# Optimization experiments

Measured on AMD Instinct MI355X. Metric: run time of the kernel, lower is better.

The kernel has to match this reference:

```python
import jax, jax.numpy as jnp
import numpy as np
from jax import lax


def _conv(x, w, b):
    # x: [B,C,H,W] NCHW, w: [O,I,3,3] OIHW, SAME padding, stride 1
    y = lax.conv_general_dilated(x, w, (1, 1), 'SAME',
                                 dimension_numbers=('NCHW', 'OIHW', 'NCHW'))
    return y + b[None, :, None, None]


def _maxpool2(x):
    return lax.reduce_window(x, -jnp.inf, lax.max,
                             (1, 1, 2, 2), (1, 1, 2, 2), 'VALID')


def _squash(x):
    # x: [..., D]
    norm = jnp.sum(x * x, axis=-1, keepdims=True)
    scale = norm / (1.0 + norm) / jnp.sqrt(norm + 1e-9)
    return scale * x


def _routing(x, W):
    # x: [B, R, C]  (R routes, C in_channels); W: [N, R, C, O]
    # u_hat[b,n,r,o] = sum_c x[b,r,c] * W[n,r,c,o]
    u_hat = jnp.einsum('brc,nrco->bnro', x, W)
    B, N, R, O = u_hat.shape
    b_ij = jnp.zeros((B, N, R), dtype=u_hat.dtype)
    v = None
    for it in range(3):  # fixed 3 routing iterations
        c_ij = jax.nn.softmax(b_ij, axis=2)
        s_j = jnp.einsum('bnr,bnro->bno', c_ij, u_hat)
        v = _squash(s_j)
        if it < 2:
            b_ij = b_ij + jnp.einsum('bnro,bno->bnr', u_hat, v)
    return v  # [B, N, O]


def setup_inputs() -> dict:
    key = jax.random.key(0)
    ks = jax.random.split(key, 10)
    B = 512
    num_classes = 15
    x = jax.random.normal(ks[0], (B, 3, 64, 64), dtype=jnp.float32)

    def kaiming(k, shape, fan_in):
        return jax.random.normal(k, shape, dtype=jnp.float32) * np.sqrt(2.0 / fan_in)

    w1 = kaiming(ks[1], (8, 3, 3, 3), 3 * 9)
    b1 = jnp.zeros((8,), jnp.float32)
    w2 = kaiming(ks[2], (16, 8, 3, 3), 8 * 9)
    b2 = jnp.zeros((16,), jnp.float32)
    w3 = kaiming(ks[3], (32, 16, 3, 3), 16 * 9)
    b3 = jnp.zeros((32,), jnp.float32)
    # route_weights are torch.randn in the original (std 1.0)
    rw1 = jax.random.normal(ks[4], (32, 64, 32, 8), dtype=jnp.float32)   # primary
    rw2 = jax.random.normal(ks[5], (num_classes, 32, 8, 16), dtype=jnp.float32)  # secondary
    fc_w = kaiming(ks[6], (num_classes, 16 * num_classes), 16 * num_classes)
    fc_b = jnp.zeros((num_classes,), jnp.float32)
    return {'x': x, 'w1': w1, 'b1': b1, 'w2': w2, 'b2': b2,
            'w3': w3, 'b3': b3, 'rw1': rw1, 'rw2': rw2,
            'fc_w': fc_w, 'fc_b': fc_b}


def reference(x, w1, b1, w2, b2, w3, b3, rw1, rw2, fc_w, fc_b):
    h = _maxpool2(jax.nn.relu(_conv(x, w1, b1)))   # [B,8,32,32]
    h = _maxpool2(jax.nn.relu(_conv(h, w2, b2)))   # [B,16,16,16]
    h = _maxpool2(jax.nn.relu(_conv(h, w3, b3)))   # [B,32,8,8]
    B = h.shape[0]
    # routes = 64 spatial positions, channels = 32 capsule input features
    feats = h.reshape(B, 32, 64).transpose(0, 2, 1)  # [B, 64, 32]
    v1 = _routing(feats, rw1)   # [B, 32, 8]
    v2 = _routing(v1, rw2)      # [B, 15, 16]
    flat = v2.reshape(B, -1)    # [B, 240]
    return flat @ fc_w.T + fc_b  # [B, 15]
```

## Files before the change

### kernel.cpp

```cpp
#include <hip/hip_runtime.h>
#include <hip/hip_bf16.h>


__global__ __launch_bounds__(256)
void conv_stack(const float* __restrict__ x,
                const float* __restrict__ w1g, const float* __restrict__ b1g,
                const float* __restrict__ w2g, const float* __restrict__ b2g,
                const float* __restrict__ w3g, const float* __restrict__ b3g,
                float* __restrict__ h3)
{
    __shared__ float lds[18152];
    float* A  = lds;
    float* o1 = lds + 6936;
    float* w3 = lds + 6936;
    float* o3 = lds + 11544;
    float* w1 = lds + 16728;
    float* w2 = lds + 16944;
    float* bb = lds + 18096;

    const int tid = threadIdx.x;
    const int b   = blockIdx.x;

    {
        float4 z = make_float4(0.f, 0.f, 0.f, 0.f);
        for (int i = tid; i < 4182; i += 256) ((float4*)lds)[i] = z;
        for (int i = tid; i < 216; i += 256) {
            int o = i % 8, k = (i / 8) % 9, c = i / 72;
            w1[i] = w1g[(o * 3 + c) * 9 + k];
        }
        for (int i = tid; i < 1152; i += 256) {
            int o = i % 16, k = (i / 16) % 9, c = i / 144;
            w2[i] = w2g[(o * 8 + c) * 9 + k];
        }
        if (tid < 8)  bb[tid]      = b1g[tid];
        if (tid < 16) bb[8 + tid]  = b2g[tid];
        if (tid < 32) bb[24 + tid] = b3g[tid];
    }
    const float4* gin = (const float4*)(x + (size_t)b * 3 * 64 * 64);

    auto stage_band = [&](int y0) {
        for (int i = tid; i < 3 * 34 * 16; i += 256) {
            int ch = i % 16;
            int ly = (i / 16) % 34;
            int c  = i / (16 * 34);
            int y  = y0 + ly;
            float4 v = make_float4(0.f, 0.f, 0.f, 0.f);
            if (y >= 0 && y < 64) v = gin[(c * 64 + y) * 16 + ch];
            float* d = &A[(c * 34 + ly) * 68 + 1 + ch * 4];
            d[0] = v.x; d[1] = v.y; d[2] = v.z; d[3] = v.w;
        }
    };
    stage_band(-1);
    __syncthreads();

    auto conv1_band = [&](int band) {
        const int s  = tid & 7;
        const int py = (tid >> 3) & 15;
        const int og = tid >> 7;
        const int X0 = 8 * s;
        float acc[4][2][8];
#pragma unroll
        for (int n = 0; n < 4; ++n)
#pragma unroll
            for (int q = 0; q < 2; ++q)
#pragma unroll
                for (int j = 0; j < 8; ++j) acc[n][q][j] = 0.f;
#pragma unroll
        for (int c = 0; c < 3; ++c) {
            float rows[4][12];
#pragma unroll
            for (int rr = 0; rr < 4; ++rr) {
                const float4* src = (const float4*)&A[(c * 34 + 2 * py + rr) * 68 + X0];
#pragma unroll
                for (int j = 0; j < 3; ++j) {
                    float4 v = src[j];
                    rows[rr][j * 4 + 0] = v.x; rows[rr][j * 4 + 1] = v.y;
                    rows[rr][j * 4 + 2] = v.z; rows[rr][j * 4 + 3] = v.w;
                }
            }
            const float* wc = w1 + c * 72;
#pragma unroll
            for (int ky = 0; ky < 3; ++ky)
#pragma unroll
                for (int n = 0; n < 4; ++n) {
                    const float q0 = wc[(ky * 3 + 0) * 8 + og * 4 + n];
                    const float q1 = wc[(ky * 3 + 1) * 8 + og * 4 + n];
                    const float q2 = wc[(ky * 3 + 2) * 8 + og * 4 + n];
#pragma unroll
                    for (int j = 0; j < 8; ++j) {
                        acc[n][0][j] = fmaf(rows[ky][j],     q0, acc[n][0][j]);
                        acc[n][0][j] = fmaf(rows[ky][j + 1], q1, acc[n][0][j]);
                        acc[n][0][j] = fmaf(rows[ky][j + 2], q2, acc[n][0][j]);
                        acc[n][1][j] = fmaf(rows[ky + 1][j],     q0, acc[n][1][j]);
                        acc[n][1][j] = fmaf(rows[ky + 1][j + 1], q1, acc[n][1][j]);
                        acc[n][1][j] = fmaf(rows[ky + 1][j + 2], q2, acc[n][1][j]);
                    }
                }
        }
#pragma unroll
        for (int n = 0; n < 4; ++n) {
            const float bv = bb[og * 4 + n];
            const int row = 1 + band * 16 + py;
#pragma unroll
            for (int j = 0; j < 4; ++j) {
                float m = fmaxf(fmaxf(acc[n][0][2 * j], acc[n][0][2 * j + 1]),
                                fmaxf(acc[n][1][2 * j], acc[n][1][2 * j + 1]));
                o1[((og * 4 + n) * 34 + row) * 36 + 1 + 4 * s + j] = fmaxf(m + bv, 0.f);
            }
        }
    };
    conv1_band(0);
    __syncthreads();
    stage_band(31);
    __syncthreads();
    conv1_band(1);
    __syncthreads();

    {
        float4 z = make_float4(0.f, 0.f, 0.f, 0.f);
        for (int i = tid; i < 1734; i += 256) ((float4*)A)[i] = z;
    }
    __syncthreads();

    {
        const int s  = tid & 3;
        const int py = (tid >> 2) & 15;
        const int og = tid >> 6;
        const int X0 = 8 * s;
        float acc[4][2][8];
#pragma unroll
        for (int n = 0; n < 4; ++n)
#pragma unroll
            for (int q = 0; q < 2; ++q)
#pragma unroll
                for (int j = 0; j < 8; ++j) acc[n][q][j] = 0.f;
        for (int c = 0; c < 8; ++c) {
            float rows[4][12];
#pragma unroll
            for (int rr = 0; rr < 4; ++rr) {
                const float4* src = (const float4*)&o1[(c * 34 + 2 * py + rr) * 36 + X0];
#pragma unroll
                for (int j = 0; j < 3; ++j) {
                    float4 v = src[j];
                    rows[rr][j * 4 + 0] = v.x; rows[rr][j * 4 + 1] = v.y;
                    rows[rr][j * 4 + 2] = v.z; rows[rr][j * 4 + 3] = v.w;
                }
            }
            const float* wc = w2 + c * 144;
#pragma unroll
            for (int ky = 0; ky < 3; ++ky)
#pragma unroll
                for (int n = 0; n < 4; ++n) {
                    const float q0 = wc[(ky * 3 + 0) * 16 + og * 4 + n];
                    const float q1 = wc[(ky * 3 + 1) * 16 + og * 4 + n];
                    const float q2 = wc[(ky * 3 + 2) * 16 + og * 4 + n];
#pragma unroll
                    for (int j = 0; j < 8; ++j) {
                        acc[n][0][j] = fmaf(rows[ky][j],     q0, acc[n][0][j]);
                        acc[n][0][j] = fmaf(rows[ky][j + 1], q1, acc[n][0][j]);
                        acc[n][0][j] = fmaf(rows[ky][j + 2], q2, acc[n][0][j]);
                        acc[n][1][j] = fmaf(rows[ky + 1][j],     q0, acc[n][1][j]);
                        acc[n][1][j] = fmaf(rows[ky + 1][j + 1], q1, acc[n][1][j]);
                        acc[n][1][j] = fmaf(rows[ky + 1][j + 2], q2, acc[n][1][j]);
                    }
                }
        }
#pragma unroll
        for (int n = 0; n < 4; ++n) {
            const float bv = bb[8 + og * 4 + n];
#pragma unroll
            for (int j = 0; j < 4; ++j) {
                float m = fmaxf(fmaxf(acc[n][0][2 * j], acc[n][0][2 * j + 1]),
                                fmaxf(acc[n][1][2 * j], acc[n][1][2 * j + 1]));
                A[((og * 4 + n) * 18 + 1 + py) * 20 + 1 + 4 * s + j] = fmaxf(m + bv, 0.f);
            }
        }
    }
    __syncthreads();

    for (int i = tid; i < 4608; i += 256) {
        int o = i % 32, k = (i / 32) % 9, c = i / 288;
        w3[i] = w3g[(o * 16 + c) * 9 + k];
    }
    __syncthreads();

    {
        const int s  = tid & 1;
        const int py = (tid >> 1) & 7;
        const int og = tid >> 4;
        const int X0 = 8 * s;
        float acc[2][2][8];
#pragma unroll
        for (int n = 0; n < 2; ++n)
#pragma unroll
            for (int q = 0; q < 2; ++q)
#pragma unroll
                for (int j = 0; j < 8; ++j) acc[n][q][j] = 0.f;
        for (int c = 0; c < 16; ++c) {
            float rows[4][12];
#pragma unroll
            for (int rr = 0; rr < 4; ++rr) {
                const float4* src = (const float4*)&A[(c * 18 + 2 * py + rr) * 20 + X0];
#pragma unroll
                for (int j = 0; j < 3; ++j) {
                    float4 v = src[j];
                    rows[rr][j * 4 + 0] = v.x; rows[rr][j * 4 + 1] = v.y;
                    rows[rr][j * 4 + 2] = v.z; rows[rr][j * 4 + 3] = v.w;
                }
            }
            const float* wc = w3 + c * 288;
#pragma unroll
            for (int ky = 0; ky < 3; ++ky)
#pragma unroll
                for (int n = 0; n < 2; ++n) {
                    const float q0 = wc[(ky * 3 + 0) * 32 + og * 2 + n];
                    const float q1 = wc[(ky * 3 + 1) * 32 + og * 2 + n];
                    const float q2 = wc[(ky * 3 + 2) * 32 + og * 2 + n];
#pragma unroll
                    for (int j = 0; j < 8; ++j) {
                        acc[n][0][j] = fmaf(rows[ky][j],     q0, acc[n][0][j]);
                        acc[n][0][j] = fmaf(rows[ky][j + 1], q1, acc[n][0][j]);
                        acc[n][0][j] = fmaf(rows[ky][j + 2], q2, acc[n][0][j]);
                        acc[n][1][j] = fmaf(rows[ky + 1][j],     q0, acc[n][1][j]);
                        acc[n][1][j] = fmaf(rows[ky + 1][j + 1], q1, acc[n][1][j]);
                        acc[n][1][j] = fmaf(rows[ky + 1][j + 2], q2, acc[n][1][j]);
                    }
                }
        }
#pragma unroll
        for (int n = 0; n < 2; ++n) {
            const float bv = bb[24 + og * 2 + n];
            float4 ov;
            float* p = (float*)&ov;
#pragma unroll
            for (int j = 0; j < 4; ++j) {
                float m = fmaxf(fmaxf(acc[n][0][2 * j], acc[n][0][2 * j + 1]),
                                fmaxf(acc[n][1][2 * j], acc[n][1][2 * j + 1]));
                p[j] = fmaxf(m + bv, 0.f);
            }
            *(float4*)&o3[(og * 2 + n) * 64 + py * 8 + 4 * s] = ov;
        }
    }
    __syncthreads();

    {
        float4* dst = (float4*)(h3 + (size_t)b * 2048);
        const float4* src = (const float4*)o3;
        for (int i = tid; i < 512; i += 256) dst[i] = src[i];
    }
}

__global__ __launch_bounds__(256)
void transpose_w1(const float* __restrict__ W, float* __restrict__ Wt)
{
    int idx = blockIdx.x * 256 + threadIdx.x;
    if (idx >= 32 * 32 * 64 * 2) return;
    int half = idx & 1;
    int r    = (idx >> 1) & 63;
    int c    = (idx >> 7) & 31;
    int n    = idx >> 12;
    ((float4*)Wt)[idx] =
        ((const float4*)W)[(((n * 64 + r) * 32 + c) << 1) + half];
}

__global__ __launch_bounds__(256)
void routing1_einsum(const float* __restrict__ h3, const float* __restrict__ Wt,
                     float* __restrict__ uhat)
{
    constexpr int C = 32, R = 64, O = 8, G = 8;
    const int lane = threadIdx.x & 63;
    const int n    = blockIdx.y * 4 + (threadIdx.x >> 6);
    const int b0   = blockIdx.x * G;

    float u[G][O];
#pragma unroll
    for (int g = 0; g < G; ++g)
#pragma unroll
        for (int o = 0; o < O; ++o) u[g][o] = 0.f;

    const float4* wp = (const float4*)Wt + (size_t)n * C * R * 2;
    const float* xb = h3 + (size_t)b0 * (C * R) + lane;

#pragma unroll 4
    for (int c = 0; c < C; ++c) {
        float xv[G];
#pragma unroll
        for (int g = 0; g < G; ++g) xv[g] = xb[(size_t)g * (C * R) + c * R];
        float4 w0 = wp[(c * R + lane) * 2];
        float4 w1 = wp[(c * R + lane) * 2 + 1];
#pragma unroll
        for (int g = 0; g < G; ++g) {
            u[g][0] = fmaf(xv[g], w0.x, u[g][0]);
            u[g][1] = fmaf(xv[g], w0.y, u[g][1]);
            u[g][2] = fmaf(xv[g], w0.z, u[g][2]);
            u[g][3] = fmaf(xv[g], w0.w, u[g][3]);
            u[g][4] = fmaf(xv[g], w1.x, u[g][4]);
            u[g][5] = fmaf(xv[g], w1.y, u[g][5]);
            u[g][6] = fmaf(xv[g], w1.z, u[g][6]);
            u[g][7] = fmaf(xv[g], w1.w, u[g][7]);
        }
    }
#pragma unroll
    for (int g = 0; g < G; ++g) {
        float4* dst = (float4*)(uhat + (((size_t)(b0 + g) * 32 + n) * R + lane) * O);
        dst[0] = make_float4(u[g][0], u[g][1], u[g][2], u[g][3]);
        dst[1] = make_float4(u[g][4], u[g][5], u[g][6], u[g][7]);
    }
}

__global__ __launch_bounds__(256)
void routing1_iter(const float* __restrict__ uhat, float* __restrict__ v1)
{
    constexpr int O = 8;
    const int t  = threadIdx.x;
    const int b  = blockIdx.x;
    const int n  = t >> 3;
    const int rp = t & 7;

    float u[8][O];
    {
        const float4* up = (const float4*)(uhat + (((size_t)b * 32 + n) * 64 + rp * 8) * O);
#pragma unroll
        for (int i = 0; i < 16; ++i) {
            float4 w = up[i];
            u[i >> 1][(i & 1) * 4 + 0] = w.x;
            u[i >> 1][(i & 1) * 4 + 1] = w.y;
            u[i >> 1][(i & 1) * 4 + 2] = w.z;
            u[i >> 1][(i & 1) * 4 + 3] = w.w;
        }
    }

    float bij[8];
#pragma unroll
    for (int k = 0; k < 8; ++k) bij[k] = 0.f;
    float s[O];

#pragma unroll
    for (int it = 0; it < 3; ++it) {
        float e[8];
        float inv;
        if (it == 0) {
#pragma unroll
            for (int k = 0; k < 8; ++k) e[k] = 1.f;
            inv = 1.0f / 64.0f;
        } else {
            float mx = bij[0];
#pragma unroll
            for (int k = 1; k < 8; ++k) mx = fmaxf(mx, bij[k]);
#pragma unroll
            for (int m = 1; m < 8; m <<= 1) mx = fmaxf(mx, __shfl_xor(mx, m, 64));
            float sum = 0.f;
#pragma unroll
            for (int k = 0; k < 8; ++k) { e[k] = __expf(bij[k] - mx); sum += e[k]; }
#pragma unroll
            for (int m = 1; m < 8; m <<= 1) sum += __shfl_xor(sum, m, 64);
            inv = 1.f / sum;
        }
        float ta[O];
#pragma unroll
        for (int o = 0; o < O; ++o) ta[o] = 0.f;
#pragma unroll
        for (int k = 0; k < 8; ++k)
#pragma unroll
            for (int o = 0; o < O; ++o) ta[o] = fmaf(e[k], u[k][o], ta[o]);
#pragma unroll
        for (int m = 1; m < 8; m <<= 1)
#pragma unroll
            for (int o = 0; o < O; ++o) ta[o] += __shfl_xor(ta[o], m, 64);
        float nr = 0.f;
#pragma unroll
        for (int o = 0; o < O; ++o) { s[o] = ta[o] * inv; nr = fmaf(s[o], s[o], nr); }
        float scale = nr / (1.f + nr) / sqrtf(nr + 1e-9f);
#pragma unroll
        for (int o = 0; o < O; ++o) s[o] *= scale;
        if (it < 2) {
#pragma unroll
            for (int k = 0; k < 8; ++k) {
                float d = 0.f;
#pragma unroll
                for (int o = 0; o < O; ++o) d = fmaf(u[k][o], s[o], d);
                bij[k] += d;
            }
        }
    }
    float outv = s[0];
#pragma unroll
    for (int o = 1; o < O; ++o) outv = (rp == o) ? s[o] : outv;
    v1[(size_t)b * 256 + n * 8 + rp] = outv;
}

__global__ __launch_bounds__(256)
void routing2_fc(const float* __restrict__ v1, const float* __restrict__ W,
                 const float* __restrict__ fcw, const float* __restrict__ fcb,
                 float* __restrict__ out)
{
    constexpr int R = 32, C = 8, O = 16;
    __shared__ float vv[240];

    const int t  = threadIdx.x;
    const int b  = blockIdx.x;
    const int wv = t >> 6;
    const int lane = t & 63;
    const int nh = lane >> 5;
    const int r  = lane & 31;

    const float4* xr = (const float4*)(v1 + (size_t)b * 256 + r * 8);
    float4 x0 = xr[0], x1 = xr[1];
    float xv[8] = {x0.x, x0.y, x0.z, x0.w, x1.x, x1.y, x1.z, x1.w};

    float u[2][O];
    int nn[2];
#pragma unroll
    for (int p = 0; p < 2; ++p) {
        int n = wv * 4 + p * 2 + nh;
        nn[p] = n;
        int ncl = n < 15 ? n : 14;
        const float4* wp = (const float4*)(W + ((size_t)(ncl * R + r) * C) * O);
#pragma unroll
        for (int o = 0; o < O; ++o) u[p][o] = 0.f;
#pragma unroll
        for (int c = 0; c < C; ++c) {
#pragma unroll
            for (int j = 0; j < 4; ++j) {
                float4 w4 = wp[c * 4 + j];
                u[p][j * 4 + 0] = fmaf(xv[c], w4.x, u[p][j * 4 + 0]);
                u[p][j * 4 + 1] = fmaf(xv[c], w4.y, u[p][j * 4 + 1]);
                u[p][j * 4 + 2] = fmaf(xv[c], w4.z, u[p][j * 4 + 2]);
                u[p][j * 4 + 3] = fmaf(xv[c], w4.w, u[p][j * 4 + 3]);
            }
        }
    }

    float bij[2] = {0.f, 0.f};
    float s[2][O];
#pragma unroll
    for (int it = 0; it < 3; ++it) {
#pragma unroll
        for (int p = 0; p < 2; ++p) {
            float cc;
            if (it == 0) {
                cc = 1.0f / 32.0f;
            } else {
                float mx = bij[p];
#pragma unroll
                for (int w = 1; w < 32; w <<= 1) mx = fmaxf(mx, __shfl_xor(mx, w, 32));
                float e = __expf(bij[p] - mx);
                float sum = e;
#pragma unroll
                for (int w = 1; w < 32; w <<= 1) sum += __shfl_xor(sum, w, 32);
                cc = e / sum;
            }
#pragma unroll
            for (int o = 0; o < O; ++o) s[p][o] = cc * u[p][o];
        }
#pragma unroll
        for (int w = 1; w < 32; w <<= 1)
#pragma unroll
            for (int p = 0; p < 2; ++p)
#pragma unroll
                for (int o = 0; o < O; ++o) s[p][o] += __shfl_xor(s[p][o], w, 32);
#pragma unroll
        for (int p = 0; p < 2; ++p) {
            float nr = 0.f;
#pragma unroll
            for (int o = 0; o < O; ++o) nr = fmaf(s[p][o], s[p][o], nr);
            float scale = nr / (1.f + nr) / sqrtf(nr + 1e-9f);
#pragma unroll
            for (int o = 0; o < O; ++o) s[p][o] *= scale;
            if (it < 2) {
                float d = 0.f;
#pragma unroll
                for (int o = 0; o < O; ++o) d = fmaf(u[p][o], s[p][o], d);
                bij[p] += d;
            }
        }
    }
#pragma unroll
    for (int p = 0; p < 2; ++p) {
        float outv = 0.f;
#pragma unroll
        for (int o = 0; o < O; ++o) outv = (r == o) ? s[p][o] : outv;
        if (r < O && nn[p] < 15) vv[nn[p] * O + r] = outv;
    }
    __syncthreads();
    if (t < 240) {
        int j = t >> 4, k0 = t & 15;
        float acc = 0.f;
        for (int k = k0; k < 240; k += 16) acc = fmaf(vv[k], fcw[j * 240 + k], acc);
#pragma unroll
        for (int w = 1; w < 16; w <<= 1) acc += __shfl_xor(acc, w, 16);
        if (k0 == 0) out[(size_t)b * 15 + j] = acc + fcb[j];
    }
}

extern "C" void kernel_launch(void* const* d_in, const int* in_sizes, int n_in,
                              void* d_out, int out_size, void* d_ws, size_t ws_size,
                              hipStream_t stream) {
    const float* x    = (const float*)d_in[0];
    const float* w1   = (const float*)d_in[1];
    const float* b1   = (const float*)d_in[2];
    const float* w2   = (const float*)d_in[3];
    const float* b2   = (const float*)d_in[4];
    const float* w3   = (const float*)d_in[5];
    const float* b3   = (const float*)d_in[6];
    const float* rw1  = (const float*)d_in[7];
    const float* rw2  = (const float*)d_in[8];
    const float* fcw  = (const float*)d_in[9];
    const float* fcb  = (const float*)d_in[10];
    float* out = (float*)d_out;

    const int B = 512;
    float* ws = (float*)d_ws;
    float* uhat = ws;
    float* h3   = uhat + (size_t)8388608;
    float* v1   = h3 + (size_t)B * 32 * 8 * 8;
    float* Wt   = v1 + (size_t)B * 256;

    conv_stack<<<B, 256, 0, stream>>>(x, w1, b1, w2, b2, w3, b3, h3);
    transpose_w1<<<(32 * 32 * 64 * 2 + 255) / 256, 256, 0, stream>>>(rw1, Wt);
    {
        dim3 grid(B / 8, 8);
        routing1_einsum<<<grid, 256, 0, stream>>>(h3, Wt, uhat);
    }
    routing1_iter<<<B, 256, 0, stream>>>(uhat, v1);
    routing2_fc<<<B, 256, 0, stream>>>(v1, rw2, fcw, fcb, out);
}
```

Before: 199.1 us.

## Split conv stack per image into two row halves with halo recompute

```diff
diff --git a/kernel.cpp b/kernel.cpp
--- a/kernel.cpp
+++ b/kernel.cpp
@@ -3,27 +3,30 @@
 
 
 __global__ __launch_bounds__(256)
-void conv_stack(const float* __restrict__ x,
-                const float* __restrict__ w1g, const float* __restrict__ b1g,
-                const float* __restrict__ w2g, const float* __restrict__ b2g,
-                const float* __restrict__ w3g, const float* __restrict__ b3g,
-                float* __restrict__ h3)
+void conv_stack_h(const float* __restrict__ x,
+                  const float* __restrict__ w1g, const float* __restrict__ b1g,
+                  const float* __restrict__ w2g, const float* __restrict__ b2g,
+                  const float* __restrict__ w3g, const float* __restrict__ b3g,
+                  float* __restrict__ h3)
 {
-    __shared__ float lds[18152];
+    __shared__ float lds[11960];
     float* A  = lds;
-    float* o1 = lds + 6936;
-    float* w3 = lds + 6936;
-    float* o3 = lds + 11544;
-    float* w1 = lds + 16728;
-    float* w2 = lds + 16944;
-    float* bb = lds + 18096;
+    float* o2 = lds;
+    float* o1 = lds + 4488;
+    float* w3 = lds + 4488;
+    float* o3 = lds + 9096;
+    float* w1 = lds + 10536;
+    float* w2 = lds + 10752;
+    float* bb = lds + 11904;
 
     const int tid = threadIdx.x;
     const int b   = blockIdx.x;
+    const int h   = blockIdx.y;
+    const int base1 = h ? 12 : -1;
 
     {
         float4 z = make_float4(0.f, 0.f, 0.f, 0.f);
-        for (int i = tid; i < 4182; i += 256) ((float4*)lds)[i] = z;
+        for (int i = tid; i < 2634; i += 256) ((float4*)lds)[i] = z;
         for (int i = tid; i < 216; i += 256) {
             int o = i % 8, k = (i / 8) % 9, c = i / 72;
             w1[i] = w1g[(o * 3 + c) * 9 + k];
@@ -36,28 +39,104 @@
         if (tid < 16) bb[8 + tid]  = b2g[tid];
         if (tid < 32) bb[24 + tid] = b3g[tid];
     }
+    __syncthreads();
+
     const float4* gin = (const float4*)(x + (size_t)b * 3 * 64 * 64);
 
-    auto stage_band = [&](int y0) {
-        for (int i = tid; i < 3 * 34 * 16; i += 256) {
-            int ch = i % 16;
-            int ly = (i / 16) % 34;
-            int c  = i / (16 * 34);
-            int y  = y0 + ly;
+    auto stage_band = [&](int x0) {
+        for (int i = tid; i < 3 * 22 * 16; i += 256) {
+            int ch = i & 15;
+            int ly = (i >> 4) % 22;
+            int c  = i / (16 * 22);
+            int y  = x0 + ly;
             float4 v = make_float4(0.f, 0.f, 0.f, 0.f);
             if (y >= 0 && y < 64) v = gin[(c * 64 + y) * 16 + ch];
-            float* d = &A[(c * 34 + ly) * 68 + 1 + ch * 4];
+            float* d = &A[(c * 22 + ly) * 68 + 1 + ch * 4];
             d[0] = v.x; d[1] = v.y; d[2] = v.z; d[3] = v.w;
         }
     };
-    stage_band(-1);
-    __syncthreads();
-
-    auto conv1_band = [&](int band) {
-        const int s  = tid & 7;
-        const int py = (tid >> 3) & 15;
-        const int og = tid >> 7;
+
+    auto conv1_band = [&](int l_start, int nrows) {
+        const int NT = nrows * 16;
+        if (tid < NT) {
+            const int s  = tid & 7;
+            const int lr = (tid >> 3) % nrows;
+            const int og = tid / (8 * nrows);
+            const int X0 = 8 * s;
+            float acc[4][2][8];
+#pragma unroll
+            for (int n = 0; n < 4; ++n)
+#pragma unroll
+                for (int q = 0; q < 2; ++q)
+#pragma unroll
+                    for (int j = 0; j < 8; ++j) acc[n][q][j] = 0.f;
+#pragma unroll
+            for (int c = 0; c < 3; ++c) {
+                float rows[4][12];
+#pragma unroll
+                for (int rr = 0; rr < 4; ++rr) {
+                    const float4* src = (const float4*)&A[(c * 22 + 2 * lr + rr) * 68 + X0];
+#pragma unroll
+                    for (int j = 0; j < 3; ++j) {
+                        float4 v = src[j];
+                        rows[rr][j * 4 + 0] = v.x; rows[rr][j * 4 + 1] = v.y;
+                        rows[rr][j * 4 + 2] = v.z; rows[rr][j * 4 + 3] = v.w;
+                    }
+                }
+                const float* wc = w1 + c * 72;
+#pragma unroll
+                for (int ky = 0; ky < 3; ++ky)
+#pragma unroll
+                    for (int n = 0; n < 4; ++n) {
+                        const float q0 = wc[(ky * 3 + 0) * 8 + og * 4 + n];
+                        const float q1 = wc[(ky * 3 + 1) * 8 + og * 4 + n];
+                        const float q2 = wc[(ky * 3 + 2) * 8 + og * 4 + n];
+#pragma unroll
+                        for (int j = 0; j < 8; ++j) {
+                            acc[n][0][j] = fmaf(rows[ky][j],     q0, acc[n][0][j]);
+                            acc[n][0][j] = fmaf(rows[ky][j + 1], q1, acc[n][0][j]);
+                            acc[n][0][j] = fmaf(rows[ky][j + 2], q2, acc[n][0][j]);
+                            acc[n][1][j] = fmaf(rows[ky + 1][j],     q0, acc[n][1][j]);
+                            acc[n][1][j] = fmaf(rows[ky + 1][j + 1], q1, acc[n][1][j]);
+                            acc[n][1][j] = fmaf(rows[ky + 1][j + 2], q2, acc[n][1][j]);
+                        }
+                    }
+            }
+            const int l = l_start + lr;
+#pragma unroll
+            for (int n = 0; n < 4; ++n) {
+                const float bv = bb[og * 4 + n];
+#pragma unroll
+                for (int j = 0; j < 4; ++j) {
+                    float m = fmaxf(fmaxf(acc[n][0][2 * j], acc[n][0][2 * j + 1]),
+                                    fmaxf(acc[n][1][2 * j], acc[n][1][2 * j + 1]));
+                    o1[((og * 4 + n) * 21 + l) * 36 + 1 + 4 * s + j] = fmaxf(m + bv, 0.f);
+                }
+            }
+        }
+    };
+
+    stage_band(2 * base1 + 1);
+    __syncthreads();
+    conv1_band(1, 10);
+    __syncthreads();
+    stage_band(2 * base1 + 21);
+    __syncthreads();
+    conv1_band(11, 9);
+    __syncthreads();
+
+    {
+        float4 z = make_float4(0.f, 0.f, 0.f, 0.f);
+        for (int i = tid; i < 800; i += 256) ((float4*)o2)[i] = z;
+    }
+    __syncthreads();
+
+    if (tid < 144) {
+        const int s  = tid & 3;
+        const int jl = (tid >> 2) % 9;
+        const int og = tid / 36;
         const int X0 = 8 * s;
+        const int l2 = jl + 1 - h;
         float acc[4][2][8];
 #pragma unroll
         for (int n = 0; n < 4; ++n)
@@ -65,12 +144,11 @@
             for (int q = 0; q < 2; ++q)
 #pragma unroll
                 for (int j = 0; j < 8; ++j) acc[n][q][j] = 0.f;
-#pragma unroll
-        for (int c = 0; c < 3; ++c) {
+        for (int c = 0; c < 8; ++c) {
             float rows[4][12];
 #pragma unroll
             for (int rr = 0; rr < 4; ++rr) {
-                const float4* src = (const float4*)&A[(c * 34 + 2 * py + rr) * 68 + X0];
+                const float4* src = (const float4*)&o1[(c * 21 + 2 * jl + h + rr) * 36 + X0];
 #pragma unroll
                 for (int j = 0; j < 3; ++j) {
                     float4 v = src[j];
@@ -78,14 +156,14 @@
                     rows[rr][j * 4 + 2] = v.z; rows[rr][j * 4 + 3] = v.w;
                 }
             }
-            const float* wc = w1 + c * 72;
+            const float* wc = w2 + c * 144;
 #pragma unroll
             for (int ky = 0; ky < 3; ++ky)
 #pragma unroll
                 for (int n = 0; n < 4; ++n) {
-                    const float q0 = wc[(ky * 3 + 0) * 8 + og * 4 + n];
-                    const float q1 = wc[(ky * 3 + 1) * 8 + og * 4 + n];
-                    const float q2 = wc[(ky * 3 + 2) * 8 + og * 4 + n];
+                    const float q0 = wc[(ky * 3 + 0) * 16 + og * 4 + n];
+                    const float q1 = wc[(ky * 3 + 1) * 16 + og * 4 + n];
+                    const float q2 = wc[(ky * 3 + 2) * 16 + og * 4 + n];
 #pragma unroll
                     for (int j = 0; j < 8; ++j) {
                         acc[n][0][j] = fmaf(rows[ky][j],     q0, acc[n][0][j]);
@@ -99,46 +177,40 @@
         }
 #pragma unroll
         for (int n = 0; n < 4; ++n) {
-            const float bv = bb[og * 4 + n];
-            const int row = 1 + band * 16 + py;
+            const float bv = bb[8 + og * 4 + n];
 #pragma unroll
             for (int j = 0; j < 4; ++j) {
                 float m = fmaxf(fmaxf(acc[n][0][2 * j], acc[n][0][2 * j + 1]),
                                 fmaxf(acc[n][1][2 * j], acc[n][1][2 * j + 1]));
-                o1[((og * 4 + n) * 34 + row) * 36 + 1 + 4 * s + j] = fmaxf(m + bv, 0.f);
-            }
-        }
-    };
-    conv1_band(0);
-    __syncthreads();
-    stage_band(31);
-    __syncthreads();
-    conv1_band(1);
-    __syncthreads();
-
-    {
-        float4 z = make_float4(0.f, 0.f, 0.f, 0.f);
-        for (int i = tid; i < 1734; i += 256) ((float4*)A)[i] = z;
-    }
-    __syncthreads();
-
-    {
-        const int s  = tid & 3;
-        const int py = (tid >> 2) & 15;
-        const int og = tid >> 6;
+                o2[((og * 4 + n) * 10 + l2) * 20 + 1 + 4 * s + j] = fmaxf(m + bv, 0.f);
+            }
+        }
+    }
+    __syncthreads();
+
+    for (int i = tid; i < 4608; i += 256) {
+        int o = i % 32, k = (i / 32) % 9, c = i / 288;
+        w3[i] = w3g[(o * 16 + c) * 9 + k];
+    }
+    __syncthreads();
+
+    if (tid < 128) {
+        const int s  = tid & 1;
+        const int k  = (tid >> 1) & 3;
+        const int og = tid >> 3;
         const int X0 = 8 * s;
-        float acc[4][2][8];
-#pragma unroll
-        for (int n = 0; n < 4; ++n)
+        float acc[2][2][8];
+#pragma unroll
+        for (int n = 0; n < 2; ++n)
 #pragma unroll
             for (int q = 0; q < 2; ++q)
 #pragma unroll
                 for (int j = 0; j < 8; ++j) acc[n][q][j] = 0.f;
-        for (int c = 0; c < 8; ++c) {
+        for (int c = 0; c < 16; ++c) {
             float rows[4][12];
 #pragma unroll
             for (int rr = 0; rr < 4; ++rr) {
-                const float4* src = (const float4*)&o1[(c * 34 + 2 * py + rr) * 36 + X0];
+                const float4* src = (const float4*)&o2[(c * 10 + 2 * k + rr) * 20 + X0];
 #pragma unroll
                 for (int j = 0; j < 3; ++j) {
                     float4 v = src[j];
@@ -146,14 +218,14 @@
                     rows[rr][j * 4 + 2] = v.z; rows[rr][j * 4 + 3] = v.w;
                 }
             }
-            const float* wc = w2 + c * 144;
+            const float* wc = w3 + c * 288;
 #pragma unroll
             for (int ky = 0; ky < 3; ++ky)
 #pragma unroll
-                for (int n = 0; n < 4; ++n) {
-                    const float q0 = wc[(ky * 3 + 0) * 16 + og * 4 + n];
-                    const float q1 = wc[(ky * 3 + 1) * 16 + og * 4 + n];
-                    const float q2 = wc[(ky * 3 + 2) * 16 + og * 4 + n];
+                for (int n = 0; n < 2; ++n) {
+                    const float q0 = wc[(ky * 3 + 0) * 32 + og * 2 + n];
+                    const float q1 = wc[(ky * 3 + 1) * 32 + og * 2 + n];
+                    const float q2 = wc[(ky * 3 + 2) * 32 + og * 2 + n];
 #pragma unroll
                     for (int j = 0; j < 8; ++j) {
                         acc[n][0][j] = fmaf(rows[ky][j],     q0, acc[n][0][j]);
@@ -166,68 +238,6 @@
                 }
         }
 #pragma unroll
-        for (int n = 0; n < 4; ++n) {
-            const float bv = bb[8 + og * 4 + n];
-#pragma unroll
-            for (int j = 0; j < 4; ++j) {
-                float m = fmaxf(fmaxf(acc[n][0][2 * j], acc[n][0][2 * j + 1]),
-                                fmaxf(acc[n][1][2 * j], acc[n][1][2 * j + 1]));
-                A[((og * 4 + n) * 18 + 1 + py) * 20 + 1 + 4 * s + j] = fmaxf(m + bv, 0.f);
-            }
-        }
-    }
-    __syncthreads();
-
-    for (int i = tid; i < 4608; i += 256) {
-        int o = i % 32, k = (i / 32) % 9, c = i / 288;
-        w3[i] = w3g[(o * 16 + c) * 9 + k];
-    }
-    __syncthreads();
-
-    {
-        const int s  = tid & 1;
-        const int py = (tid >> 1) & 7;
-        const int og = tid >> 4;
-        const int X0 = 8 * s;
-        float acc[2][2][8];
-#pragma unroll
-        for (int n = 0; n < 2; ++n)
-#pragma unroll
-            for (int q = 0; q < 2; ++q)
-#pragma unroll
-                for (int j = 0; j < 8; ++j) acc[n][q][j] = 0.f;
-        for (int c = 0; c < 16; ++c) {
-            float rows[4][12];
-#pragma unroll
-            for (int rr = 0; rr < 4; ++rr) {
-                const float4* src = (const float4*)&A[(c * 18 + 2 * py + rr) * 20 + X0];
-#pragma unroll
-                for (int j = 0; j < 3; ++j) {
-                    float4 v = src[j];
-                    rows[rr][j * 4 + 0] = v.x; rows[rr][j * 4 + 1] = v.y;
-                    rows[rr][j * 4 + 2] = v.z; rows[rr][j * 4 + 3] = v.w;
-                }
-            }
-            const float* wc = w3 + c * 288;
-#pragma unroll
-            for (int ky = 0; ky < 3; ++ky)
-#pragma unroll
-                for (int n = 0; n < 2; ++n) {
-                    const float q0 = wc[(ky * 3 + 0) * 32 + og * 2 + n];
-                    const float q1 = wc[(ky * 3 + 1) * 32 + og * 2 + n];
-                    const float q2 = wc[(ky * 3 + 2) * 32 + og * 2 + n];
-#pragma unroll
-                    for (int j = 0; j < 8; ++j) {
-                        acc[n][0][j] = fmaf(rows[ky][j],     q0, acc[n][0][j]);
-                        acc[n][0][j] = fmaf(rows[ky][j + 1], q1, acc[n][0][j]);
-                        acc[n][0][j] = fmaf(rows[ky][j + 2], q2, acc[n][0][j]);
-                        acc[n][1][j] = fmaf(rows[ky + 1][j],     q0, acc[n][1][j]);
-                        acc[n][1][j] = fmaf(rows[ky + 1][j + 1], q1, acc[n][1][j]);
-                        acc[n][1][j] = fmaf(rows[ky + 1][j + 2], q2, acc[n][1][j]);
-                    }
-                }
-        }
-#pragma unroll
         for (int n = 0; n < 2; ++n) {
             const float bv = bb[24 + og * 2 + n];
             float4 ov;
@@ -238,15 +248,18 @@
                                 fmaxf(acc[n][1][2 * j], acc[n][1][2 * j + 1]));
                 p[j] = fmaxf(m + bv, 0.f);
             }
-            *(float4*)&o3[(og * 2 + n) * 64 + py * 8 + 4 * s] = ov;
+            *(float4*)&o3[(og * 2 + n) * 32 + k * 8 + 4 * s] = ov;
         }
     }
     __syncthreads();
 
     {
-        float4* dst = (float4*)(h3 + (size_t)b * 2048);
+        const int ch = tid >> 3;
+        const int k  = (tid >> 1) & 3;
+        const int cq = tid & 1;
         const float4* src = (const float4*)o3;
-        for (int i = tid; i < 512; i += 256) dst[i] = src[i];
+        float4* dst = (float4*)(h3 + (size_t)b * 2048 + ch * 64 + (4 * h + k) * 8 + cq * 4);
+        *dst = src[tid];
     }
 }
 
@@ -516,7 +529,7 @@
     float* v1   = h3 + (size_t)B * 32 * 8 * 8;
     float* Wt   = v1 + (size_t)B * 256;
 
-    conv_stack<<<B, 256, 0, stream>>>(x, w1, b1, w2, b2, w3, b3, h3);
+    conv_stack_h<<<dim3(B, 2), 256, 0, stream>>>(x, w1, b1, w2, b2, w3, b3, h3);
     transpose_w1<<<(32 * 32 * 64 * 2 + 255) / 256, 256, 0, stream>>>(rw1, Wt);
     {
         dim3 grid(B / 8, 8);
```

Result: slower. 219.2 us (+10.1%).
